# Kernel optimization log

Measured on AMD Instinct MI355X. Metric: run time of the kernel, lower is better.

The kernel has to match this reference:

```python
import jax, jax.numpy as jnp
import numpy as np
from jax import lax

VOCAB, EMB, HID, NCLS = 30000, 256, 256, 10


def setup_inputs() -> dict:
    key = jax.random.key(0)
    ks = jax.random.split(key, 12)
    B, T = 128, 512
    s_e = 1.0 / np.sqrt(EMB)
    s_h = 1.0 / np.sqrt(HID)
    inp = {
        "inputs": jax.random.randint(ks[0], (B, T), 0, VOCAB),
        "emb_table": jax.random.normal(ks[1], (VOCAB, EMB), jnp.float32),
        # forward-direction GRU params (torch layout: gates ordered r,z,n)
        "W_ih_f": jax.random.uniform(ks[2], (3 * HID, EMB), jnp.float32, -s_h, s_h),
        "W_hh_f": jax.random.uniform(ks[3], (3 * HID, HID), jnp.float32, -s_h, s_h),
        "b_ih_f": jax.random.uniform(ks[4], (3 * HID,), jnp.float32, -s_h, s_h),
        "b_hh_f": jax.random.uniform(ks[5], (3 * HID,), jnp.float32, -s_h, s_h),
        # backward-direction GRU params
        "W_ih_b": jax.random.uniform(ks[6], (3 * HID, EMB), jnp.float32, -s_h, s_h),
        "W_hh_b": jax.random.uniform(ks[7], (3 * HID, HID), jnp.float32, -s_h, s_h),
        "b_ih_b": jax.random.uniform(ks[8], (3 * HID,), jnp.float32, -s_h, s_h),
        "b_hh_b": jax.random.uniform(ks[9], (3 * HID,), jnp.float32, -s_h, s_h),
        # classifier head
        "W_lin": jax.random.uniform(ks[10], (NCLS, 2 * HID), jnp.float32, -1.0 / np.sqrt(2 * HID), 1.0 / np.sqrt(2 * HID)),
        "b_lin": jax.random.uniform(ks[11], (NCLS,), jnp.float32, -1.0 / np.sqrt(2 * HID), 1.0 / np.sqrt(2 * HID)),
    }
    return inp


def _gru_dir(x_tbe, W_ih, W_hh, b_ih, b_hh):
    """Run GRU over time-major x [T,B,E]; returns final hidden [B,H]."""
    # Precompute input projections for all steps in one big GEMM.
    xg = jnp.einsum("tbe,ge->tbg", x_tbe, W_ih) + b_ih  # [T,B,3H]

    def step(h, xg_t):
        hg = h @ W_hh.T + b_hh  # [B,3H]
        xr, xz, xn = jnp.split(xg_t, 3, axis=-1)
        hr, hz, hn = jnp.split(hg, 3, axis=-1)
        r = jax.nn.sigmoid(xr + hr)
        z = jax.nn.sigmoid(xz + hz)
        n = jnp.tanh(xn + r * hn)
        h_new = (1.0 - z) * n + z * h
        return h_new, None

    h0 = jnp.zeros((x_tbe.shape[1], W_hh.shape[1]), x_tbe.dtype)
    h_last, _ = lax.scan(step, h0, xg)
    return h_last


def reference(inputs, emb_table, W_ih_f, W_hh_f, b_ih_f, b_hh_f,
              W_ih_b, W_hh_b, b_ih_b, b_hh_b, W_lin, b_lin):
    # Dropout is identity in eval mode.
    emb = emb_table[inputs]               # [B,T,E]
    x = jnp.transpose(emb, (1, 0, 2))     # time-major [T,B,E]
    h_f = _gru_dir(x, W_ih_f, W_hh_f, b_ih_f, b_hh_f)            # [B,H]
    h_b = _gru_dir(x[::-1], W_ih_b, W_hh_b, b_ih_b, b_hh_b)      # [B,H]
    hidden = jnp.concatenate([h_f, h_b], axis=-1)                 # [B,2H]
    return hidden @ W_lin.T + b_lin                               # [B,10]
```

## Files before the change

### kernel.cpp

```cpp
#include <hip/hip_runtime.h>


typedef float f32x4 __attribute__((ext_vector_type(4)));
typedef short s16x8 __attribute__((ext_vector_type(8)));

#define VOCAB   30000
#define GCOLS   1536
#define HB_STR  280
#define HBUF    (16 * HB_STR)
#define GP_STR  1032
#define HS_STR  260
#define SRF     (-1.4426950408889634f)
#define SNF     (2.8853900817779268f)

#if defined(__has_builtin)
#if __has_builtin(__builtin_amdgcn_cvt_pk_bf16_f32)
#define HAVE_PK 1
#endif
#endif

static __device__ __forceinline__ unsigned short f2bf(float f) {
    unsigned u = __builtin_bit_cast(unsigned, f);
    u += 0x7fffu + ((u >> 16) & 1u);
    return (unsigned short)(u >> 16);
}
#ifdef HAVE_PK
typedef __bf16 bf16x2_t __attribute__((ext_vector_type(2)));
static __device__ __forceinline__ unsigned pk2(float a, float b) {
    bf16x2_t v = __builtin_amdgcn_cvt_pk_bf16_f32(a, b);
    return __builtin_bit_cast(unsigned, v);
}
#else
static __device__ __forceinline__ unsigned pk2(float a, float b) {
    return (unsigned)f2bf(a) | ((unsigned)f2bf(b) << 16);
}
#endif
static __device__ __forceinline__ float bf_lo(unsigned v) {
    return __builtin_bit_cast(float, v << 16);
}
static __device__ __forceinline__ float bf_hi(unsigned v) {
    return __builtin_bit_cast(float, v & 0xffff0000u);
}
static __device__ __forceinline__ s16x8 pack_bf8(float4 a, float4 b, float s) {
    union { s16x8 v; unsigned u[4]; } r;
    r.u[0] = pk2(a.x * s, a.y * s); r.u[1] = pk2(a.z * s, a.w * s);
    r.u[2] = pk2(b.x * s, b.y * s); r.u[3] = pk2(b.z * s, b.w * s);
    return r.v;
}
static __device__ __forceinline__ f32x4 mfma16(s16x8 a, s16x8 b, f32x4 c) {
    return __builtin_amdgcn_mfma_f32_16x16x32_bf16(a, b, c, 0, 0, 0);
}
static __device__ __forceinline__ float sig2(float x) {
    return __builtin_amdgcn_rcpf(1.0f + __builtin_amdgcn_exp2f(x));
}
static __device__ __forceinline__ void gload_lds16(const unsigned short* g, unsigned short* l) {
    __builtin_amdgcn_global_load_lds(
        (const __attribute__((address_space(1))) unsigned*)g,
        (__attribute__((address_space(3))) unsigned*)l, 16, 0, 0);
}

__global__ __launch_bounds__(512, 2)
void gru_table_kernel(const float* __restrict__ emb,
                      const float* __restrict__ Wih_f, const float* __restrict__ bih_f,
                      const float* __restrict__ bhh_f,
                      const float* __restrict__ Wih_b, const float* __restrict__ bih_b,
                      const float* __restrict__ bhh_b,
                      unsigned short* __restrict__ G) {
    __shared__ unsigned short aS[16 * HB_STR];
    const int tid  = threadIdx.x;
    const int lane = tid & 63;
    const int w    = tid >> 6;
    const int u    = lane & 15;
    const int q    = lane >> 4;
    const int strip = blockIdx.x;
    const int by    = blockIdx.y;

    s16x8 breg[2][8];
    float beta[2];
    int   ntg_j[2];
#pragma unroll
    for (int j = 0; j < 2; ++j) {
        int ntg = strip * 16 + w * 2 + j;
        ntg_j[j] = ntg;
        int dd = (ntg >= 48) ? 1 : 0;
        int tl = ntg - dd * 48;
        int wp = tl / 6;
        int t  = tl - wp * 6;
        int orig = (t >> 1) * 256 + 32 * wp + ((t & 1) << 4) + u;
        const float* Wih = dd ? Wih_b : Wih_f;
        const float* bih = dd ? bih_b : bih_f;
        const float* bhh = dd ? bhh_b : bhh_f;
        const float scl = (t < 4) ? SRF : SNF;
        beta[j] = (bih[orig] + ((t < 4) ? bhh[orig] : 0.0f)) * scl;
#pragma unroll
        for (int kt = 0; kt < 8; ++kt) {
            const float* p = Wih + orig * 256 + kt * 32 + q * 8;
            float4 x0 = *(const float4*)p;
            float4 x1 = *(const float4*)(p + 4);
            breg[j][kt] = pack_bf8(x0, x1, scl);
        }
    }

    for (int mt = 0; mt < 32; ++mt) {
        const int v0 = by * 512 + mt * 16;
        {
            int row = tid >> 5;
            int c8  = (tid & 31) * 8;
            int v   = v0 + row;
            float4 e0 = make_float4(0.f, 0.f, 0.f, 0.f), e1 = e0;
            if (v < VOCAB) {
                const float* p = emb + (size_t)v * 256 + c8;
                e0 = *(const float4*)p;
                e1 = *(const float4*)(p + 4);
            }
            unsigned* dp = (unsigned*)&aS[row * HB_STR + c8];
            dp[0] = pk2(e0.x, e0.y); dp[1] = pk2(e0.z, e0.w);
            dp[2] = pk2(e1.x, e1.y); dp[3] = pk2(e1.z, e1.w);
        }
        __syncthreads();

        f32x4 acc0 = {0.f, 0.f, 0.f, 0.f}, acc1 = acc0;
#pragma unroll
        for (int kt = 0; kt < 8; ++kt) {
            s16x8 af = *(const s16x8*)&aS[u * HB_STR + kt * 32 + q * 8];
            acc0 = mfma16(af, breg[0][kt], acc0);
            acc1 = mfma16(af, breg[1][kt], acc1);
        }
#pragma unroll
        for (int j = 0; j < 2; ++j) {
            f32x4 a = j ? acc1 : acc0;
#pragma unroll
            for (int r = 0; r < 4; ++r) {
                int v = v0 + q * 4 + r;
                if (v < VOCAB)
                    G[(size_t)v * GCOLS + ntg_j[j] * 16 + u] = f2bf(a[r] + beta[j]);
            }
        }
        __syncthreads();
    }
}

__global__ __launch_bounds__(512, 2)
void gru_rnn_kernel(const int* __restrict__ inp,
                    const float* __restrict__ Whh_f, const float* __restrict__ bhh_f,
                    const float* __restrict__ Whh_b, const float* __restrict__ bhh_b,
                    const float* __restrict__ W_lin, const float* __restrict__ b_lin,
                    const unsigned short* __restrict__ G,
                    float* __restrict__ out) {
    __shared__ int            toks[16][513];
    __shared__ unsigned short hB[2 * HBUF];
    __shared__ unsigned short xgS[2][16][GP_STR];
    __shared__ float          bhnS[256];
    __shared__ float          hs[16 * HS_STR];

    const int tid  = threadIdx.x;
    const int lane = tid & 63;
    const int w    = tid >> 6;
    const int b    = lane & 15;
    const int q    = lane >> 4;
    const int d    = blockIdx.x >> 3;
    const int b0   = (blockIdx.x & 7) * 16;

    const float* Whh = d ? Whh_b : Whh_f;
    const float* bhh = d ? bhh_b : bhh_f;

    s16x8 wreg[48];
#pragma unroll
    for (int t = 0; t < 6; ++t) {
        const int orig = (t >> 1) * 256 + 32 * w + ((t & 1) << 4) + b;
        const float scl = (t < 4) ? SRF : SNF;
#pragma unroll
        for (int kt = 0; kt < 8; ++kt) {
            const float* p = Whh + orig * 256 + kt * 32 + q * 8;
            wreg[t * 8 + kt] =
                pack_bf8(*(const float4*)p, *(const float4*)(p + 4), scl);
        }
    }

    for (int i = tid; i < 16 * 512; i += 512) {
        int bb = i >> 9, t = i & 511;
        toks[bb][t] = inp[(b0 + bb) * 512 + t];
    }
    for (int i = tid; i < 2 * HBUF; i += 512) hB[i] = 0;
    if (tid < 256) bhnS[tid] = SNF * bhh[512 + tid];
    __syncthreads();

    {
        int t0 = d ? 511 : 0;
#pragma unroll
        for (int j = 0; j < 2; ++j) {
            int bb = 2 * w + j;
            int tok = toks[bb][t0];
            const unsigned short* gb = G + (size_t)tok * GCOLS + (d ? 512 : 0) + lane * 8;
            gload_lds16(gb,       &xgS[0][bb][0]);
            gload_lds16(gb + 512, &xgS[0][bb][512]);
        }
    }
    __syncthreads();

    const int xoff = d ? 256 : 0;
    const int hbq  = b * HB_STR + q * 8;
    float hreg[8];
#pragma unroll
    for (int i = 0; i < 8; ++i) hreg[i] = 0.f;

#pragma unroll 2
    for (int ts = 0; ts < 512; ++ts) {
        const int rb = (ts & 1) * HBUF;
        const int pn = (ts + 1) & 1;
        {
            int s1 = (ts < 511) ? ts + 1 : 511;
            int t1 = d ? 511 - s1 : s1;
#pragma unroll
            for (int j = 0; j < 2; ++j) {
                int bb = 2 * w + j;
                int tok = toks[bb][t1];
                const unsigned short* gb = G + (size_t)tok * GCOLS + (d ? 512 : 0) + lane * 8;
                gload_lds16(gb,       &xgS[pn][bb][0]);
                gload_lds16(gb + 512, &xgS[pn][bb][512]);
            }
        }
#pragma unroll
        for (int l = 0; l < 2; ++l) {
            f32x4 ar = {0.f, 0.f, 0.f, 0.f};
            f32x4 az = {0.f, 0.f, 0.f, 0.f};
            f32x4 an = *(const f32x4*)&bhnS[32 * w + 16 * l + 4 * q];
#pragma unroll
            for (int kt = 0; kt < 8; ++kt) {
                s16x8 hf = *(const s16x8*)&hB[rb + hbq + kt * 32];
                ar = mfma16(wreg[(0 + l) * 8 + kt], hf, ar);
                az = mfma16(wreg[(2 + l) * 8 + kt], hf, az);
                an = mfma16(wreg[(4 + l) * 8 + kt], hf, an);
            }
            const unsigned short* xrow = &xgS[ts & 1][b][xoff + 96 * w + 16 * l + 4 * q];
            uint2 uxr = *(const uint2*)&xrow[0];
            uint2 uxz = *(const uint2*)&xrow[32];
            uint2 uxn = *(const uint2*)&xrow[64];
            float xr[4] = {bf_lo(uxr.x), bf_hi(uxr.x), bf_lo(uxr.y), bf_hi(uxr.y)};
            float xz[4] = {bf_lo(uxz.x), bf_hi(uxz.x), bf_lo(uxz.y), bf_hi(uxz.y)};
            float xn[4] = {bf_lo(uxn.x), bf_hi(uxn.x), bf_lo(uxn.y), bf_hi(uxn.y)};
#pragma unroll
            for (int r = 0; r < 4; ++r) {
                float rg = sig2(xr[r] + ar[r]);
                float zg = sig2(xz[r] + az[r]);
                float tg = sig2(fmaf(rg, an[r], xn[r]));
                float ng = fmaf(-2.0f, tg, 1.0f);
                const int i = l * 4 + r;
                hreg[i] = fmaf(zg, hreg[i] - ng, ng);
            }
            unsigned p0 = pk2(hreg[l * 4 + 0], hreg[l * 4 + 1]);
            unsigned p1 = pk2(hreg[l * 4 + 2], hreg[l * 4 + 3]);
            *(uint2*)&hB[pn * HBUF + b * HB_STR + 32 * w + 16 * l + 4 * q] =
                make_uint2(p0, p1);
        }
        __syncthreads();
    }

#pragma unroll
    for (int l = 0; l < 2; ++l) {
        f32x4 v = {hreg[l * 4 + 0], hreg[l * 4 + 1],
                   hreg[l * 4 + 2], hreg[l * 4 + 3]};
        *(f32x4*)&hs[b * HS_STR + 32 * w + 16 * l + 4 * q] = v;
    }
    __syncthreads();
    if (tid < 160) {
        int bb = tid / 10;
        int c  = tid - bb * 10;
        float acc = d ? 0.0f : b_lin[c];
        const float* wl = W_lin + c * 512 + d * 256;
        const float* hp = &hs[bb * HS_STR];
        for (int i = 0; i < 256; ++i) acc += hp[i] * wl[i];
        atomicAdd(&out[(b0 + bb) * 10 + c], acc);
    }
}

extern "C" void kernel_launch(void* const* d_in, const int* in_sizes, int n_in,
                              void* d_out, int out_size, void* d_ws, size_t ws_size,
                              hipStream_t stream) {
    const int*   inp   = (const int*)d_in[0];
    const float* emb   = (const float*)d_in[1];
    const float* Wih_f = (const float*)d_in[2];
    const float* Whh_f = (const float*)d_in[3];
    const float* bih_f = (const float*)d_in[4];
    const float* bhh_f = (const float*)d_in[5];
    const float* Wih_b = (const float*)d_in[6];
    const float* Whh_b = (const float*)d_in[7];
    const float* bih_b = (const float*)d_in[8];
    const float* bhh_b = (const float*)d_in[9];
    const float* W_lin = (const float*)d_in[10];
    const float* b_lin = (const float*)d_in[11];
    float* out = (float*)d_out;
    unsigned short* G = (unsigned short*)d_ws;

    hipMemsetAsync(d_out, 0, (size_t)out_size * sizeof(float), stream);
    hipLaunchKernelGGL(gru_table_kernel, dim3(6, 60), dim3(512), 0, stream,
                       emb, Wih_f, bih_f, bhh_f, Wih_b, bih_b, bhh_b, G);
    hipLaunchKernelGGL(gru_rnn_kernel, dim3(16), dim3(512), 0, stream,
                       inp, Whh_f, bhh_f, Whh_b, bhh_b, W_lin, b_lin, G, out);
}
```

Before: 1.095 ms.

## Restructure vocab-table GEMM to load embeddings directly into registers with wider N tiles

The table kernel drops its shared-memory staging and per-tile barriers. Each lane now loads its embedding rows straight from global memory into MFMA A fragments, and each wave computes four N-tiles instead of two over a 3x80 grid that strides through the vocabulary. The recurrent kernel stores token ids pre-multiplied by the row stride and seeds the r/z accumulators with the precomputed input projections, which removes index math and adds from the serial per-step path. In exchange the table kernel holds more weight registers and makes uncoalesced per-lane global loads, and it drops the vocab bound check because the vocabulary splits exactly into the tile count.

```diff
diff --git a/kernel.cpp b/kernel.cpp
--- a/kernel.cpp
+++ b/kernel.cpp
@@ -47,6 +47,12 @@
     r.u[2] = pk2(b.x * s, b.y * s); r.u[3] = pk2(b.z * s, b.w * s);
     return r.v;
 }
+static __device__ __forceinline__ s16x8 pack_bf8_ns(float4 a, float4 b) {
+    union { s16x8 v; unsigned u[4]; } r;
+    r.u[0] = pk2(a.x, a.y); r.u[1] = pk2(a.z, a.w);
+    r.u[2] = pk2(b.x, b.y); r.u[3] = pk2(b.z, b.w);
+    return r.v;
+}
 static __device__ __forceinline__ f32x4 mfma16(s16x8 a, s16x8 b, f32x4 c) {
     return __builtin_amdgcn_mfma_f32_16x16x32_bf16(a, b, c, 0, 0, 0);
 }
@@ -58,6 +64,7 @@
         (const __attribute__((address_space(1))) unsigned*)g,
         (__attribute__((address_space(3))) unsigned*)l, 16, 0, 0);
 }
+
 
 __global__ __launch_bounds__(512, 2)
 void gru_table_kernel(const float* __restrict__ emb,
@@ -66,21 +73,19 @@
                       const float* __restrict__ Wih_b, const float* __restrict__ bih_b,
                       const float* __restrict__ bhh_b,
                       unsigned short* __restrict__ G) {
-    __shared__ unsigned short aS[16 * HB_STR];
-    const int tid  = threadIdx.x;
-    const int lane = tid & 63;
-    const int w    = tid >> 6;
+    const int lane = threadIdx.x & 63;
+    const int w    = threadIdx.x >> 6;
     const int u    = lane & 15;
     const int q    = lane >> 4;
     const int strip = blockIdx.x;
     const int by    = blockIdx.y;
 
-    s16x8 breg[2][8];
-    float beta[2];
-    int   ntg_j[2];
-#pragma unroll
-    for (int j = 0; j < 2; ++j) {
-        int ntg = strip * 16 + w * 2 + j;
+    s16x8 breg[4][8];
+    float beta[4];
+    int   ntg_j[4];
+#pragma unroll
+    for (int j = 0; j < 4; ++j) {
+        int ntg = strip * 32 + w * 4 + j;
         ntg_j[j] = ntg;
         int dd = (ntg >= 48) ? 1 : 0;
         int tl = ntg - dd * 48;
@@ -95,48 +100,32 @@
 #pragma unroll
         for (int kt = 0; kt < 8; ++kt) {
             const float* p = Wih + orig * 256 + kt * 32 + q * 8;
-            float4 x0 = *(const float4*)p;
-            float4 x1 = *(const float4*)(p + 4);
-            breg[j][kt] = pack_bf8(x0, x1, scl);
-        }
-    }
-
-    for (int mt = 0; mt < 32; ++mt) {
-        const int v0 = by * 512 + mt * 16;
-        {
-            int row = tid >> 5;
-            int c8  = (tid & 31) * 8;
-            int v   = v0 + row;
-            float4 e0 = make_float4(0.f, 0.f, 0.f, 0.f), e1 = e0;
-            if (v < VOCAB) {
-                const float* p = emb + (size_t)v * 256 + c8;
-                e0 = *(const float4*)p;
-                e1 = *(const float4*)(p + 4);
-            }
-            unsigned* dp = (unsigned*)&aS[row * HB_STR + c8];
-            dp[0] = pk2(e0.x, e0.y); dp[1] = pk2(e0.z, e0.w);
-            dp[2] = pk2(e1.x, e1.y); dp[3] = pk2(e1.z, e1.w);
-        }
-        __syncthreads();
-
-        f32x4 acc0 = {0.f, 0.f, 0.f, 0.f}, acc1 = acc0;
+            breg[j][kt] = pack_bf8(*(const float4*)p, *(const float4*)(p + 4), scl);
+        }
+    }
+
+    for (int mt = by; mt < 1875; mt += 80) {
+        const int v0 = mt * 16;
+        const float* arow = emb + (size_t)(v0 + u) * 256 + q * 8;
+        f32x4 a0 = {0.f, 0.f, 0.f, 0.f}, a1 = a0, a2 = a0, a3 = a0;
 #pragma unroll
         for (int kt = 0; kt < 8; ++kt) {
-            s16x8 af = *(const s16x8*)&aS[u * HB_STR + kt * 32 + q * 8];
-            acc0 = mfma16(af, breg[0][kt], acc0);
-            acc1 = mfma16(af, breg[1][kt], acc1);
-        }
-#pragma unroll
-        for (int j = 0; j < 2; ++j) {
-            f32x4 a = j ? acc1 : acc0;
-#pragma unroll
-            for (int r = 0; r < 4; ++r) {
-                int v = v0 + q * 4 + r;
-                if (v < VOCAB)
-                    G[(size_t)v * GCOLS + ntg_j[j] * 16 + u] = f2bf(a[r] + beta[j]);
-            }
-        }
-        __syncthreads();
+            float4 x0 = *(const float4*)(arow + kt * 32);
+            float4 x1 = *(const float4*)(arow + kt * 32 + 4);
+            s16x8 af = pack_bf8_ns(x0, x1);
+            a0 = mfma16(af, breg[0][kt], a0);
+            a1 = mfma16(af, breg[1][kt], a1);
+            a2 = mfma16(af, breg[2][kt], a2);
+            a3 = mfma16(af, breg[3][kt], a3);
+        }
+#pragma unroll
+        for (int j = 0; j < 4; ++j) {
+            f32x4 a = (j == 0) ? a0 : (j == 1) ? a1 : (j == 2) ? a2 : a3;
+#pragma unroll
+            for (int r = 0; r < 4; ++r)
+                G[(size_t)(v0 + q * 4 + r) * GCOLS + ntg_j[j] * 16 + u] =
+                    f2bf(a[r] + beta[j]);
+        }
     }
 }
 
@@ -179,19 +168,20 @@
 
     for (int i = tid; i < 16 * 512; i += 512) {
         int bb = i >> 9, t = i & 511;
-        toks[bb][t] = inp[(b0 + bb) * 512 + t];
+        toks[bb][t] = inp[(b0 + bb) * 512 + t] * GCOLS;
     }
     for (int i = tid; i < 2 * HBUF; i += 512) hB[i] = 0;
     if (tid < 256) bhnS[tid] = SNF * bhh[512 + tid];
     __syncthreads();
 
+    const int dcol = (d ? 512 : 0) + lane * 8;
+
     {
         int t0 = d ? 511 : 0;
 #pragma unroll
         for (int j = 0; j < 2; ++j) {
             int bb = 2 * w + j;
-            int tok = toks[bb][t0];
-            const unsigned short* gb = G + (size_t)tok * GCOLS + (d ? 512 : 0) + lane * 8;
+            const unsigned short* gb = G + toks[bb][t0] + dcol;
             gload_lds16(gb,       &xgS[0][bb][0]);
             gload_lds16(gb + 512, &xgS[0][bb][512]);
         }
@@ -214,17 +204,21 @@
 #pragma unroll
             for (int j = 0; j < 2; ++j) {
                 int bb = 2 * w + j;
-                int tok = toks[bb][t1];
-                const unsigned short* gb = G + (size_t)tok * GCOLS + (d ? 512 : 0) + lane * 8;
+                const unsigned short* gb = G + toks[bb][t1] + dcol;
                 gload_lds16(gb,       &xgS[pn][bb][0]);
                 gload_lds16(gb + 512, &xgS[pn][bb][512]);
             }
         }
 #pragma unroll
         for (int l = 0; l < 2; ++l) {
-            f32x4 ar = {0.f, 0.f, 0.f, 0.f};
-            f32x4 az = {0.f, 0.f, 0.f, 0.f};
+            const unsigned short* xrow = &xgS[ts & 1][b][xoff + 96 * w + 16 * l + 4 * q];
+            uint2 uxr = *(const uint2*)&xrow[0];
+            uint2 uxz = *(const uint2*)&xrow[32];
+            uint2 uxn = *(const uint2*)&xrow[64];
+            f32x4 ar = {bf_lo(uxr.x), bf_hi(uxr.x), bf_lo(uxr.y), bf_hi(uxr.y)};
+            f32x4 az = {bf_lo(uxz.x), bf_hi(uxz.x), bf_lo(uxz.y), bf_hi(uxz.y)};
             f32x4 an = *(const f32x4*)&bhnS[32 * w + 16 * l + 4 * q];
+            float xn[4] = {bf_lo(uxn.x), bf_hi(uxn.x), bf_lo(uxn.y), bf_hi(uxn.y)};
 #pragma unroll
             for (int kt = 0; kt < 8; ++kt) {
                 s16x8 hf = *(const s16x8*)&hB[rb + hbq + kt * 32];
@@ -232,17 +226,10 @@
                 az = mfma16(wreg[(2 + l) * 8 + kt], hf, az);
                 an = mfma16(wreg[(4 + l) * 8 + kt], hf, an);
             }
-            const unsigned short* xrow = &xgS[ts & 1][b][xoff + 96 * w + 16 * l + 4 * q];
-            uint2 uxr = *(const uint2*)&xrow[0];
-            uint2 uxz = *(const uint2*)&xrow[32];
-            uint2 uxn = *(const uint2*)&xrow[64];
-            float xr[4] = {bf_lo(uxr.x), bf_hi(uxr.x), bf_lo(uxr.y), bf_hi(uxr.y)};
-            float xz[4] = {bf_lo(uxz.x), bf_hi(uxz.x), bf_lo(uxz.y), bf_hi(uxz.y)};
-            float xn[4] = {bf_lo(uxn.x), bf_hi(uxn.x), bf_lo(uxn.y), bf_hi(uxn.y)};
 #pragma unroll
             for (int r = 0; r < 4; ++r) {
-                float rg = sig2(xr[r] + ar[r]);
-                float zg = sig2(xz[r] + az[r]);
+                float rg = sig2(ar[r]);
+                float zg = sig2(az[r]);
                 float tg = sig2(fmaf(rg, an[r], xn[r]));
                 float ng = fmaf(-2.0f, tg, 1.0f);
                 const int i = l * 4 + r;
@@ -293,7 +280,7 @@
     unsigned short* G = (unsigned short*)d_ws;
 
     hipMemsetAsync(d_out, 0, (size_t)out_size * sizeof(float), stream);
-    hipLaunchKernelGGL(gru_table_kernel, dim3(6, 60), dim3(512), 0, stream,
+    hipLaunchKernelGGL(gru_table_kernel, dim3(3, 80), dim3(512), 0, stream,
                        emb, Wih_f, bih_f, bhh_f, Wih_b, bih_b, bhh_b, G);
     hipLaunchKernelGGL(gru_rnn_kernel, dim3(16), dim3(512), 0, stream,
                        inp, Whh_f, bhh_f, Whh_b, bhh_b, W_lin, b_lin, G, out);
```

Result: slower. 1.304 ms (+19.2%).

## Restructure vocab projection table kernel: per-direction blocks with double-buffered embedding tiles

Applied to the files above, without the earlier changes.

The table kernel now assigns one GRU direction per block column, so each warp holds all six gate tiles (48 bf16 B fragments) in registers. Each embedding tile is therefore loaded once per direction instead of once per column strip. Tiles of 16 vocab rows are distributed grid-stride over 128 blocks, and the next tile is prefetched into a second LDS buffer while the current one is multiplied. The larger weight register footprint may cause spills or lower occupancy under the launch bound. The whole table build is still small next to the sequential RNN kernel, so end-to-end gains are limited.

```diff
diff --git a/kernel.cpp b/kernel.cpp
--- a/kernel.cpp
+++ b/kernel.cpp
@@ -59,6 +59,7 @@
         (__attribute__((address_space(3))) unsigned*)l, 16, 0, 0);
 }
 
+
 __global__ __launch_bounds__(512, 2)
 void gru_table_kernel(const float* __restrict__ emb,
                       const float* __restrict__ Wih_f, const float* __restrict__ bih_f,
@@ -66,75 +67,88 @@
                       const float* __restrict__ Wih_b, const float* __restrict__ bih_b,
                       const float* __restrict__ bhh_b,
                       unsigned short* __restrict__ G) {
-    __shared__ unsigned short aS[16 * HB_STR];
+    __shared__ unsigned short aS[2][16 * HB_STR];
+
     const int tid  = threadIdx.x;
     const int lane = tid & 63;
     const int w    = tid >> 6;
     const int u    = lane & 15;
     const int q    = lane >> 4;
-    const int strip = blockIdx.x;
-    const int by    = blockIdx.y;
-
-    s16x8 breg[2][8];
-    float beta[2];
-    int   ntg_j[2];
-#pragma unroll
-    for (int j = 0; j < 2; ++j) {
-        int ntg = strip * 16 + w * 2 + j;
-        ntg_j[j] = ntg;
-        int dd = (ntg >= 48) ? 1 : 0;
-        int tl = ntg - dd * 48;
-        int wp = tl / 6;
-        int t  = tl - wp * 6;
-        int orig = (t >> 1) * 256 + 32 * wp + ((t & 1) << 4) + u;
-        const float* Wih = dd ? Wih_b : Wih_f;
-        const float* bih = dd ? bih_b : bih_f;
-        const float* bhh = dd ? bhh_b : bhh_f;
+    const int d    = blockIdx.x;
+    const int by   = blockIdx.y;
+
+    const float* Wih = d ? Wih_b : Wih_f;
+    const float* bih = d ? bih_b : bih_f;
+    const float* bhh = d ? bhh_b : bhh_f;
+
+    s16x8 breg[48];
+    float beta[6];
+#pragma unroll
+    for (int t = 0; t < 6; ++t) {
+        const int orig = (t >> 1) * 256 + 32 * w + ((t & 1) << 4) + u;
         const float scl = (t < 4) ? SRF : SNF;
-        beta[j] = (bih[orig] + ((t < 4) ? bhh[orig] : 0.0f)) * scl;
+        beta[t] = (bih[orig] + ((t < 4) ? bhh[orig] : 0.0f)) * scl;
 #pragma unroll
         for (int kt = 0; kt < 8; ++kt) {
             const float* p = Wih + orig * 256 + kt * 32 + q * 8;
-            float4 x0 = *(const float4*)p;
-            float4 x1 = *(const float4*)(p + 4);
-            breg[j][kt] = pack_bf8(x0, x1, scl);
-        }
-    }
-
-    for (int mt = 0; mt < 32; ++mt) {
-        const int v0 = by * 512 + mt * 16;
-        {
-            int row = tid >> 5;
-            int c8  = (tid & 31) * 8;
-            int v   = v0 + row;
-            float4 e0 = make_float4(0.f, 0.f, 0.f, 0.f), e1 = e0;
-            if (v < VOCAB) {
-                const float* p = emb + (size_t)v * 256 + c8;
-                e0 = *(const float4*)p;
-                e1 = *(const float4*)(p + 4);
-            }
-            unsigned* dp = (unsigned*)&aS[row * HB_STR + c8];
+            breg[t * 8 + kt] =
+                pack_bf8(*(const float4*)p, *(const float4*)(p + 4), scl);
+        }
+    }
+
+    const int srow = tid >> 5;
+    const int sc8  = (tid & 31) * 8;
+
+    {
+        const float* p = emb + (size_t)(by * 16 + srow) * 256 + sc8;
+        float4 e0 = *(const float4*)p, e1 = *(const float4*)(p + 4);
+        unsigned* dp = (unsigned*)&aS[0][srow * HB_STR + sc8];
+        dp[0] = pk2(e0.x, e0.y); dp[1] = pk2(e0.z, e0.w);
+        dp[2] = pk2(e1.x, e1.y); dp[3] = pk2(e1.z, e1.w);
+    }
+    __syncthreads();
+
+    const size_t colbase = (size_t)(d * 48 + 6 * w) * 16 + u;
+
+    for (int i = 0;; ++i) {
+        const int mt = by + i * 128;
+        if (mt >= 1875) break;
+        const int mtn = mt + 128;
+        const bool has_next = (mtn < 1875);
+        const int buf = i & 1;
+
+        float4 e0, e1;
+        if (has_next) {
+            const float* p = emb + (size_t)(mtn * 16 + srow) * 256 + sc8;
+            e0 = *(const float4*)p;
+            e1 = *(const float4*)(p + 4);
+        }
+
+        const int v0 = mt * 16;
+#pragma unroll
+        for (int l = 0; l < 2; ++l) {
+            f32x4 a0 = {0.f, 0.f, 0.f, 0.f}, a1 = a0, a2 = a0;
+#pragma unroll
+            for (int kt = 0; kt < 8; ++kt) {
+                s16x8 af = *(const s16x8*)&aS[buf][u * HB_STR + kt * 32 + q * 8];
+                a0 = mfma16(af, breg[(0 + l) * 8 + kt], a0);
+                a1 = mfma16(af, breg[(2 + l) * 8 + kt], a1);
+                a2 = mfma16(af, breg[(4 + l) * 8 + kt], a2);
+            }
+#pragma unroll
+            for (int g = 0; g < 3; ++g) {
+                const f32x4 a = (g == 0) ? a0 : (g == 1) ? a1 : a2;
+                const int t = 2 * g + l;
+                unsigned short* gp = G + (size_t)(v0 + q * 4) * GCOLS + colbase + t * 16;
+#pragma unroll
+                for (int r = 0; r < 4; ++r)
+                    gp[(size_t)r * GCOLS] = f2bf(a[r] + beta[t]);
+            }
+        }
+        if (has_next) {
+            unsigned* dp = (unsigned*)&aS[buf ^ 1][srow * HB_STR + sc8];
             dp[0] = pk2(e0.x, e0.y); dp[1] = pk2(e0.z, e0.w);
             dp[2] = pk2(e1.x, e1.y); dp[3] = pk2(e1.z, e1.w);
-        }
-        __syncthreads();
-
-        f32x4 acc0 = {0.f, 0.f, 0.f, 0.f}, acc1 = acc0;
-#pragma unroll
-        for (int kt = 0; kt < 8; ++kt) {
-            s16x8 af = *(const s16x8*)&aS[u * HB_STR + kt * 32 + q * 8];
-            acc0 = mfma16(af, breg[0][kt], acc0);
-            acc1 = mfma16(af, breg[1][kt], acc1);
-        }
-#pragma unroll
-        for (int j = 0; j < 2; ++j) {
-            f32x4 a = j ? acc1 : acc0;
-#pragma unroll
-            for (int r = 0; r < 4; ++r) {
-                int v = v0 + q * 4 + r;
-                if (v < VOCAB)
-                    G[(size_t)v * GCOLS + ntg_j[j] * 16 + u] = f2bf(a[r] + beta[j]);
-            }
         }
         __syncthreads();
     }
@@ -293,7 +307,7 @@
     unsigned short* G = (unsigned short*)d_ws;
 
     hipMemsetAsync(d_out, 0, (size_t)out_size * sizeof(float), stream);
-    hipLaunchKernelGGL(gru_table_kernel, dim3(6, 60), dim3(512), 0, stream,
+    hipLaunchKernelGGL(gru_table_kernel, dim3(2, 128), dim3(512), 0, stream,
                        emb, Wih_f, bih_f, bhh_f, Wih_b, bih_b, bhh_b, G);
     hipLaunchKernelGGL(gru_rnn_kernel, dim3(16), dim3(512), 0, stream,
                        inp, Whh_f, bhh_f, Whh_b, bhh_b, W_lin, b_lin, G, out);
```

After: 1.075 ms. About the same (-1.8%).
